# Optimization experiments

Hardware: AMD Instinct MI355X
Metric: run time of the kernel (lower is better)

Reference implementation:

```python
import jax, jax.numpy as jnp
import numpy as np

N_NODES = 100000
N_EDGES = 1600000
H = 64
EPS_SM = 1e-16
NEG_SLOPE = 0.01  # LeakyReLU default
BN_EPS = 1e-5


def leaky_relu(x):
    return jnp.where(x >= 0, x, NEG_SLOPE * x)


def transformer_conv(x, src, tgt, edge_attr, Wq, bq, Wk, bk, Wv, bv, We, Ws, bs):
    # PyG TransformerConv, heads=1, concat=True, root_weight=True, lin_edge bias=False
    n = x.shape[0]
    q = x @ Wq + bq            # [N,H]
    k = x @ Wk + bk            # [N,H]
    v = x @ Wv + bv            # [N,H]
    e = edge_attr @ We         # [E,H]
    ke = k[src] + e            # [E,H]
    score = jnp.sum(q[tgt] * ke, axis=-1) / jnp.sqrt(jnp.float32(H))  # [E]
    # segment softmax over incoming edges of each target node
    m = jax.ops.segment_max(score, tgt, num_segments=n)
    m = jnp.where(jnp.isfinite(m), m, 0.0)
    p = jnp.exp(score - m[tgt])
    denom = jax.ops.segment_sum(p, tgt, num_segments=n)
    alpha = p / (denom[tgt] + EPS_SM)
    msg = (v[src] + e) * alpha[:, None]                  # [E,H]
    out = jax.ops.segment_sum(msg, tgt, num_segments=n)  # [N,H]
    return out + x @ Ws + bs


def batch_norm(x, gamma, beta):
    mean = jnp.mean(x, axis=0)
    var = jnp.mean((x - mean) ** 2, axis=0)
    return (x - mean) / jnp.sqrt(var + BN_EPS) * gamma + beta


def setup_inputs() -> dict:
    key = jax.random.key(0)
    ks = jax.random.split(key, 24)
    s = 0.05
    d = {
        "x": jax.random.normal(ks[0], (N_NODES, 2), jnp.float32),
        "edge_index": jax.random.randint(ks[1], (2, N_EDGES), 0, N_NODES, jnp.int32),
        "edge_attr": jax.random.normal(ks[2], (N_EDGES, 2), jnp.float32),
        "mask": jax.random.uniform(ks[3], (N_NODES,), jnp.float32),
        # gcn1 (in=2)
        "Wq1": jax.random.normal(ks[4], (2, H)) * s, "bq1": jnp.zeros((H,)),
        "Wk1": jax.random.normal(ks[5], (2, H)) * s, "bk1": jnp.zeros((H,)),
        "Wv1": jax.random.normal(ks[6], (2, H)) * s, "bv1": jnp.zeros((H,)),
        "We1": jax.random.normal(ks[7], (2, H)) * s,
        "Ws1": jax.random.normal(ks[8], (2, H)) * s, "bs1": jnp.zeros((H,)),
        # gcn2 (in=64)
        "Wq2": jax.random.normal(ks[9], (H, H)) * s, "bq2": jnp.zeros((H,)),
        "Wk2": jax.random.normal(ks[10], (H, H)) * s, "bk2": jnp.zeros((H,)),
        "Wv2": jax.random.normal(ks[11], (H, H)) * s, "bv2": jnp.zeros((H,)),
        "We2": jax.random.normal(ks[12], (2, H)) * s,
        "Ws2": jax.random.normal(ks[13], (H, H)) * s, "bs2": jnp.zeros((H,)),
        # batch norm
        "bn_gamma": jnp.ones((H,)), "bn_beta": jnp.zeros((H,)),
        # final MLP 64->32->1
        "Wf1": jax.random.normal(ks[14], (H, 32)) * s, "bf1": jnp.zeros((32,)),
        "Wf2": jax.random.normal(ks[15], (32, 1)) * s, "bf2": jnp.zeros((1,)),
        "iterations": 3,
    }
    return d


def reference(x, edge_index, edge_attr, mask,
              Wq1, bq1, Wk1, bk1, Wv1, bv1, We1, Ws1, bs1,
              Wq2, bq2, Wk2, bk2, Wv2, bv2, We2, Ws2, bs2,
              bn_gamma, bn_beta, Wf1, bf1, Wf2, bf2, iterations):
    src, tgt = edge_index[0], edge_index[1]
    h = transformer_conv(x, src, tgt, edge_attr, Wq1, bq1, Wk1, bk1, Wv1, bv1, We1, Ws1, bs1)
    h = leaky_relu(batch_norm(h, bn_gamma, bn_beta))
    h = leaky_relu(transformer_conv(h, src, tgt, edge_attr, Wq2, bq2, Wk2, bk2, Wv2, bv2, We2, Ws2, bs2))
    for _ in range(iterations - 1):
        h = leaky_relu(transformer_conv(h, src, tgt, edge_attr, Wq2, bq2, Wk2, bk2, Wv2, bv2, We2, Ws2, bs2))
    out = jnp.squeeze(leaky_relu(h @ Wf1 + bf1) @ Wf2 + bf2, axis=-1)  # [N]
    return out * mask
```

## Files before the change

### kernel.cpp

```cpp
#include <hip/hip_runtime.h>
#include <hip/hip_fp16.h>

#define N_NODES 100000
#define N_EDGES 1600000
#define SCAN_B ((N_NODES + 1023) / 1024)
#define BSHIFT 7
#define NB_BKT ((N_NODES + 127) / 128)
#define BCAP 2560

typedef _Float16 half2_t __attribute__((ext_vector_type(2)));
typedef _Float16 half8_t __attribute__((ext_vector_type(8)));
typedef float f32x4 __attribute__((ext_vector_type(4)));

__device__ __forceinline__ float lrelu(float x) { return x >= 0.f ? x : 0.01f * x; }

__global__ void k_count(const int* __restrict__ tgt, int* __restrict__ deg) {
    int i = blockIdx.x * 256 + threadIdx.x;
    atomicAdd(&deg[tgt[i]], 1);
}

__global__ void k_scan1(const int* __restrict__ deg, int* __restrict__ bsum) {
    __shared__ int s[256];
    int t = threadIdx.x;
    int gi = blockIdx.x * 1024 + t * 4;
    int v = 0;
    if (gi < N_NODES) {
        int4 d = *(const int4*)&deg[gi];
        v = d.x + d.y + d.z + d.w;
    }
    s[t] = v;
    __syncthreads();
    for (int d = 128; d > 0; d >>= 1) {
        if (t < d) s[t] += s[t + d];
        __syncthreads();
    }
    if (t == 0) bsum[blockIdx.x] = s[0];
}

__global__ void k_scan2(int* bsum, int* rowptr) {
    if (threadIdx.x == 0) {
        int run = 0;
        for (int b = 0; b < SCAN_B; b++) {
            int v = bsum[b];
            bsum[b] = run;
            run += v;
        }
        rowptr[N_NODES] = run;
    }
}

__global__ void k_scan3(const int* __restrict__ deg, const int* __restrict__ bsum,
                        int* __restrict__ rowptr, int* __restrict__ fill) {
    __shared__ int s[256];
    int t = threadIdx.x;
    int gi = blockIdx.x * 1024 + t * 4;
    int4 d = make_int4(0, 0, 0, 0);
    if (gi < N_NODES) d = *(const int4*)&deg[gi];
    int tsum = d.x + d.y + d.z + d.w;
    s[t] = tsum;
    __syncthreads();
    for (int dd = 1; dd < 256; dd <<= 1) {
        int val = (t >= dd) ? s[t - dd] : 0;
        __syncthreads();
        s[t] += val;
        __syncthreads();
    }
    int texcl = s[t] - tsum + bsum[blockIdx.x];
    if (gi < N_NODES) {
        int4 w;
        w.x = texcl;
        w.y = texcl + d.x;
        w.z = texcl + d.x + d.y;
        w.w = texcl + d.x + d.y + d.z;
        *(int4*)&rowptr[gi] = w;
        *(int4*)&fill[gi] = w;
    }
}

__global__ void k_scatter(const int* __restrict__ src, const int* __restrict__ tgt,
                          const float2* __restrict__ ea,
                          int* __restrict__ fill, int2* __restrict__ csr) {
    int i = blockIdx.x * 256 + threadIdx.x;
    int t = tgt[i];
    float2 e = ea[i];
    int pos = atomicAdd(&fill[t], 1);
    __half2 h2 = __floats2half2_rn(e.x, e.y);
    csr[pos] = make_int2(src[i], *(int*)&h2);
}

__global__ __launch_bounds__(256) void k_bin1(const int* __restrict__ src,
                                              const int* __restrict__ tgt,
                                              const float2* __restrict__ ea,
                                              int* __restrict__ gCur,
                                              int2* __restrict__ bin) {
    __shared__ int hist[NB_BKT];
    __shared__ int cur[NB_BKT];
    int tid = threadIdx.x;
    for (int b = tid; b < NB_BKT; b += 256) hist[b] = 0;
    __syncthreads();
    int base = blockIdx.x * 6400;
#pragma unroll 5
    for (int k = 0; k < 25; k++) {
        int i = base + k * 256 + tid;
        atomicAdd(&hist[tgt[i] >> BSHIFT], 1);
    }
    __syncthreads();
    for (int b = tid; b < NB_BKT; b += 256)
        cur[b] = atomicAdd(&gCur[b], hist[b]);
    __syncthreads();
    for (int k = 0; k < 25; k++) {
        int i = base + k * 256 + tid;
        int t = tgt[i];
        int b = t >> BSHIFT;
        float2 e = ea[i];
        int pos = atomicAdd(&cur[b], 1);
        if (pos < BCAP) {
            __half2 h2 = __floats2half2_rn(e.x, e.y);
            int2 rec;
            rec.x = src[i] | ((t & 127) << 20);
            rec.y = *(int*)&h2;
            bin[(size_t)b * BCAP + pos] = rec;
        }
    }
}

__global__ __launch_bounds__(256) void k_bin2(const int* __restrict__ gCnt,
                                              const int2* __restrict__ bin,
                                              int2* __restrict__ csr,
                                              int* __restrict__ fill) {
    __shared__ int cnt[128];
    int tid = threadIdx.x;
    if (tid < 128) cnt[tid] = 0;
    __syncthreads();
    int b = blockIdx.x;
    int nb = min(gCnt[b], BCAP);
    const int2* myb = &bin[(size_t)b * BCAP];
    for (int i = tid; i < nb; i += 256) {
        int2 rec = myb[i];
        int tloc = (rec.x >> 20) & 127;
        int s = rec.x & 0xFFFFF;
        int pos = atomicAdd(&cnt[tloc], 1);
        if (pos < 64) {
            int node = (b << BSHIFT) + tloc;
            csr[((size_t)node << 6) + pos] = make_int2(s | (rec.x & 0xFFF00000), rec.y);
        }
    }
    __syncthreads();
    if (tid < 128) {
        int node = (b << BSHIFT) + tid;
        if (node < N_NODES) fill[node] = min(cnt[tid], 64);
    }
}

__global__ void k_prep2(const float* __restrict__ Wq, const float* __restrict__ Wk,
                        const float* __restrict__ Ws, const float* __restrict__ We,
                        const float* __restrict__ bk, float* __restrict__ Wcomb) {
    int idx = blockIdx.x * 256 + threadIdx.x;
    if (idx >= 9216) return;
    int j = idx / 144;
    int m = idx - j * 144;
    float v = 0.f;
    if (m < 64) {
        float s = 0.f;
        for (int ch = 0; ch < 64; ch++) s += Wq[j * 64 + ch] * Wk[m * 64 + ch];
        v = 0.125f * s;
    } else if (m < 128) {
        v = Ws[j * 64 + (m - 64)];
    } else if (m == 128) {
        float s = 0.f;
        for (int ch = 0; ch < 64; ch++) s += Wq[j * 64 + ch] * bk[ch];
        v = 0.125f * s;
    } else if (m <= 130) {
        float s = 0.f;
        for (int ch = 0; ch < 64; ch++) s += Wq[j * 64 + ch] * We[(m - 129) * 64 + ch];
        v = 0.125f * s;
    }
    Wcomb[idx] = v;
}

__global__ void k_prepb(const float* __restrict__ Wk2, const float* __restrict__ We2,
                        const float* __restrict__ bq2, const float* __restrict__ bk2,
                        const float* __restrict__ bs2, const float* __restrict__ Wq1,
                        const float* __restrict__ Wk1, const float* __restrict__ We1,
                        const float* __restrict__ bq1, const float* __restrict__ bk1,
                        float* __restrict__ bcomb) {
    int t = threadIdx.x;
    if (t >= 160) return;
    float v = 0.f;
    if (t < 64) {
        float s = 0.f;
        for (int i = 0; i < 64; i++) s += Wk2[t * 64 + i] * bq2[i];
        v = 0.125f * s;
    } else if (t < 128) {
        v = bs2[t - 64];
    } else if (t == 128) {
        float s = 0.f;
        for (int i = 0; i < 64; i++) s += bq2[i] * bk2[i];
        v = 0.125f * s;
    } else if (t <= 130) {
        float s = 0.f;
        for (int i = 0; i < 64; i++) s += bq2[i] * We2[(t - 129) * 64 + i];
        v = 0.125f * s;
    } else if (t < 144) {
        v = 0.f;
    } else {
        int t2 = t - 144;
        float s = 0.f;
        if (t2 < 4) {
            int j = t2 >> 1, m = t2 & 1;
            for (int ch = 0; ch < 64; ch++) s += Wq1[j * 64 + ch] * Wk1[m * 64 + ch];
        } else if (t2 < 6) {
            int j = t2 - 4;
            for (int ch = 0; ch < 64; ch++) s += Wq1[j * 64 + ch] * bk1[ch];
        } else if (t2 < 8) {
            int m = t2 - 6;
            for (int ch = 0; ch < 64; ch++) s += bq1[ch] * Wk1[m * 64 + ch];
        } else if (t2 == 8) {
            for (int ch = 0; ch < 64; ch++) s += bq1[ch] * bk1[ch];
        } else if (t2 < 13) {
            int j = (t2 - 9) >> 1, d = (t2 - 9) & 1;
            for (int ch = 0; ch < 64; ch++) s += Wq1[j * 64 + ch] * We1[d * 64 + ch];
        } else if (t2 < 15) {
            int d = t2 - 13;
            for (int ch = 0; ch < 64; ch++) s += bq1[ch] * We1[d * 64 + ch];
        }
        v = 0.125f * s;
    }
    bcomb[t] = v;
}

__global__ void k_prepw(const float* __restrict__ Wcomb, __half* __restrict__ wp) {
    int t = blockIdx.x * 256 + threadIdx.x;
    if (t >= 9216) return;
    int e = t & 7;
    int lane = (t >> 3) & 63;
    int kh = (t >> 9) & 1;
    int fm = t >> 10;
    int k = (kh << 5) + ((lane >> 4) << 3) + e;
    int c = fm * 16 + (lane & 15);
    wp[t] = __float2half(Wcomb[k * 144 + c]);
}

__global__ void k_prepv(const float* __restrict__ Wv, __half* __restrict__ wvp) {
    int t = blockIdx.x * 256 + threadIdx.x;
    if (t >= 4096) return;
    int e = t & 7;
    int lane = (t >> 3) & 63;
    int kh = (t >> 9) & 1;
    int fm = t >> 10;
    int k = (kh << 5) + ((lane >> 4) << 3) + e;
    int c = fm * 16 + (lane & 15);
    wvp[t] = __float2half(Wv[k * 64 + c]);
}

__global__ __launch_bounds__(256) void k_agg1(
    const float* __restrict__ x, const int* __restrict__ idx,
    const int2* __restrict__ csr, const float* __restrict__ Wv,
    const float* __restrict__ We, const float* __restrict__ Ws,
    const float* __restrict__ bv, const float* __restrict__ bs,
    const float* __restrict__ prep, float* __restrict__ o, int bucket) {
    int node = blockIdx.x * 4 + (threadIdx.x >> 6);
    int lane = threadIdx.x & 63;
    float2 xt = *(const float2*)&x[(size_t)node << 1];
    float a0 = xt.x * prep[0] + xt.y * prep[2] + prep[6];
    float a1 = xt.x * prep[1] + xt.y * prep[3] + prep[7];
    float b1 = xt.x * prep[4] + xt.y * prep[5] + prep[8];
    float g0 = xt.x * prep[9] + xt.y * prep[11] + prep[13];
    float g1 = xt.x * prep[10] + xt.y * prep[12] + prep[14];

    float l = 0.f, px0 = 0.f, px1 = 0.f, pA = 0.f, pB = 0.f;
    if (bucket) {
        int deg = idx[node];
        bool valid = lane < deg;
        int2 rec = valid ? csr[((size_t)node << 6) + lane] : make_int2(0, 0);
        int src = rec.x & 0xFFFFF;
        float2 ef = __half22float2(*(__half2*)&rec.y);
        float2 xs = valid ? *(const float2*)&x[(size_t)src << 1] : make_float2(0.f, 0.f);
        float t = a0 * xs.x + a1 * xs.y + b1 + g0 * ef.x + g1 * ef.y;
        float pp = valid ? __expf(t) : 0.f;
        l = pp;
        px0 = pp * xs.x;
        px1 = pp * xs.y;
        pA = pp * ef.x;
        pB = pp * ef.y;
    } else {
        int beg = idx[node], end = idx[node + 1];
        for (int p = beg + lane; p < end; p += 64) {
            int2 rec = csr[p];
            float2 ef = __half22float2(*(__half2*)&rec.y);
            float2 xs = *(const float2*)&x[(size_t)rec.x << 1];
            float t = a0 * xs.x + a1 * xs.y + b1 + g0 * ef.x + g1 * ef.y;
            float pp = __expf(t);
            l += pp;
            px0 += pp * xs.x;
            px1 += pp * xs.y;
            pA += pp * ef.x;
            pB += pp * ef.y;
        }
    }
#pragma unroll
    for (int D = 1; D < 64; D <<= 1) {
        l += __shfl_xor(l, D, 64);
        px0 += __shfl_xor(px0, D, 64);
        px1 += __shfl_xor(px1, D, 64);
        pA += __shfl_xor(pA, D, 64);
        pB += __shfl_xor(pB, D, 64);
    }
    float inv = 1.f / (l + 1e-16f);
    int c = lane;
    float r = (px0 * Wv[c] + px1 * Wv[64 + c] + pA * We[c] + pB * We[64 + c] +
               l * bv[c]) * inv +
              xt.x * Ws[c] + xt.y * Ws[64 + c] + bs[c];
    o[((size_t)node << 6) + c] = r;
}

__global__ void k_bnp(const float* __restrict__ o, float* __restrict__ bnsum,
                      float* __restrict__ bnsq) {
    __shared__ float s1[256], s2[256];
    int t = threadIdx.x;
    int c = t & 63, nsub = t >> 6;
    float su = 0.f, sq = 0.f;
    int base = blockIdx.x * 400;
    for (int i = 0; i < 100; i++) {
        int node = base + i * 4 + nsub;
        float v = o[((size_t)node << 6) + c];
        su += v;
        sq += v * v;
    }
    s1[t] = su;
    s2[t] = sq;
    __syncthreads();
    if (t < 64) {
        float a = s1[t] + s1[t + 64] + s1[t + 128] + s1[t + 192];
        float b = s2[t] + s2[t + 64] + s2[t + 128] + s2[t + 192];
        atomicAdd(&bnsum[t], a);
        atomicAdd(&bnsq[t], b);
    }
}

__global__ void k_bnf(const float* bnsum, const float* bnsq, const float* gamma,
                      const float* beta, float* bnab) {
    int c = threadIdx.x;
    float mean = bnsum[c] * (1.f / N_NODES);
    float var = bnsq[c] * (1.f / N_NODES) - mean * mean;
    float A = gamma[c] * rsqrtf(var + 1e-5f);
    bnab[c] = A;
    bnab[64 + c] = beta[c] - mean * A;
}

__global__ void k_bna(const float* __restrict__ o, const float* __restrict__ bnab,
                      float* __restrict__ h, __half* __restrict__ hh) {
    int idx = blockIdx.x * 256 + threadIdx.x;
    int c = idx & 63;
    float v = lrelu(o[idx] * bnab[c] + bnab[64 + c]);
    h[idx] = v;
    hh[idx] = __float2half(v);
}

__device__ __forceinline__ half8_t pack8(float4 lo, float4 hi) {
    half8_t r;
    r[0] = (_Float16)lo.x; r[1] = (_Float16)lo.y;
    r[2] = (_Float16)lo.z; r[3] = (_Float16)lo.w;
    r[4] = (_Float16)hi.x; r[5] = (_Float16)hi.y;
    r[6] = (_Float16)hi.z; r[7] = (_Float16)hi.w;
    return r;
}

__global__ __launch_bounds__(256) void k_gemm(
    const float* __restrict__ h, const __half* __restrict__ hhin,
    const __half* __restrict__ wp, const float* __restrict__ bcomb,
    const float* __restrict__ bnab, int use_bn,
    __half* __restrict__ qh, float* __restrict__ ext, float* __restrict__ o,
    __half* __restrict__ hhout) {
    int tid = threadIdx.x;
    int w = tid >> 6;
    int lane = tid & 63;
    int nloc = lane & 15;
    int kg = lane >> 4;
    int base = blockIdx.x * 64;
    int fm0 = w << 1;

    half8_t A[2][2], AE[2];
    const half8_t* wpv = (const half8_t*)wp;
#pragma unroll
    for (int fml = 0; fml < 2; fml++)
#pragma unroll
        for (int kh = 0; kh < 2; kh++)
            A[fml][kh] = wpv[(((fm0 + fml) << 1) + kh) * 64 + lane];
    if (w == 3) {
#pragma unroll
        for (int kh = 0; kh < 2; kh++) AE[kh] = wpv[((8 << 1) + kh) * 64 + lane];
    }

    half8_t z8;
#pragma unroll
    for (int i = 0; i < 8; i++) z8[i] = (_Float16)0.f;

    half8_t B[4][2];
    int n[4];
    bool g[4];
#pragma unroll
    for (int nf = 0; nf < 4; nf++) {
        n[nf] = base + (nf << 4) + nloc;
        g[nf] = n[nf] < N_NODES;
    }

    if (use_bn) {
        float4 bnA[2][2], bnB[2][2];
#pragma unroll
        for (int kh = 0; kh < 2; kh++) {
            int k0 = (kh << 5) + (kg << 3);
            bnA[kh][0] = *(const float4*)&bnab[k0];
            bnA[kh][1] = *(const float4*)&bnab[k0 + 4];
            bnB[kh][0] = *(const float4*)&bnab[64 + k0];
            bnB[kh][1] = *(const float4*)&bnab[64 + k0 + 4];
        }
        const float4 z4 = make_float4(0.f, 0.f, 0.f, 0.f);
#pragma unroll
        for (int nf = 0; nf < 4; nf++) {
            const float* hrow = h + ((size_t)n[nf] << 6);
#pragma unroll
            for (int kh = 0; kh < 2; kh++) {
                int k0 = (kh << 5) + (kg << 3);
                float4 lo = g[nf] ? *(const float4*)&hrow[k0] : z4;
                float4 hi = g[nf] ? *(const float4*)&hrow[k0 + 4] : z4;
                lo.x = lrelu(lo.x * bnA[kh][0].x + bnB[kh][0].x);
                lo.y = lrelu(lo.y * bnA[kh][0].y + bnB[kh][0].y);
                lo.z = lrelu(lo.z * bnA[kh][0].z + bnB[kh][0].z);
                lo.w = lrelu(lo.w * bnA[kh][0].w + bnB[kh][0].w);
                hi.x = lrelu(hi.x * bnA[kh][1].x + bnB[kh][1].x);
                hi.y = lrelu(hi.y * bnA[kh][1].y + bnB[kh][1].y);
                hi.z = lrelu(hi.z * bnA[kh][1].z + bnB[kh][1].z);
                hi.w = lrelu(hi.w * bnA[kh][1].w + bnB[kh][1].w);
                B[nf][kh] = pack8(lo, hi);
                if (g[nf]) *(half8_t*)&hhout[((size_t)n[nf] << 6) + k0] = B[nf][kh];
            }
        }
        __syncthreads();
    } else {
#pragma unroll
        for (int nf = 0; nf < 4; nf++) {
#pragma unroll
            for (int kh = 0; kh < 2; kh++) {
                int k0 = (kh << 5) + (kg << 3);
                B[nf][kh] = g[nf] ? *(const half8_t*)&hhin[((size_t)n[nf] << 6) + k0]
                                  : z8;
            }
        }
    }

    f32x4 acc[4][2], accE[4];
#pragma unroll
    for (int nf = 0; nf < 4; nf++) {
        acc[nf][0] = (f32x4){0.f, 0.f, 0.f, 0.f};
        acc[nf][1] = (f32x4){0.f, 0.f, 0.f, 0.f};
        accE[nf] = (f32x4){0.f, 0.f, 0.f, 0.f};
    }

#pragma unroll
    for (int nf = 0; nf < 4; nf++) {
#pragma unroll
        for (int fml = 0; fml < 2; fml++) {
            acc[nf][fml] = __builtin_amdgcn_mfma_f32_16x16x32_f16(
                A[fml][0], B[nf][0], acc[nf][fml], 0, 0, 0);
            acc[nf][fml] = __builtin_amdgcn_mfma_f32_16x16x32_f16(
                A[fml][1], B[nf][1], acc[nf][fml], 0, 0, 0);
        }
    }
    if (w == 3) {
#pragma unroll
        for (int nf = 0; nf < 4; nf++) {
            accE[nf] = __builtin_amdgcn_mfma_f32_16x16x32_f16(AE[0], B[nf][0],
                                                              accE[nf], 0, 0, 0);
            accE[nf] = __builtin_amdgcn_mfma_f32_16x16x32_f16(AE[1], B[nf][1],
                                                              accE[nf], 0, 0, 0);
        }
    }

    int rowg = kg << 2;
#pragma unroll
    for (int fml = 0; fml < 2; fml++) {
        int fm = fm0 + fml;
        float4 bi = *(const float4*)&bcomb[fm * 16 + rowg];
#pragma unroll
        for (int nf = 0; nf < 4; nf++) {
            if (!g[nf]) continue;
            float4 r;
            r.x = acc[nf][fml][0] + bi.x;
            r.y = acc[nf][fml][1] + bi.y;
            r.z = acc[nf][fml][2] + bi.z;
            r.w = acc[nf][fml][3] + bi.w;
            if (fm < 4) {
                __half2 p0 = __floats2half2_rn(r.x, r.y);
                __half2 p1 = __floats2half2_rn(r.z, r.w);
                *(int2*)&qh[((size_t)n[nf] << 6) + fm * 16 + rowg] =
                    make_int2(*(int*)&p0, *(int*)&p1);
            } else {
                *(float4*)&o[((size_t)n[nf] << 6) + (fm - 4) * 16 + rowg] = r;
            }
        }
    }
    if (w == 3 && kg == 0) {
        float4 bi = *(const float4*)&bcomb[128];
#pragma unroll
        for (int nf = 0; nf < 4; nf++) {
            if (!g[nf]) continue;
            float4 r;
            r.x = accE[nf][0] + bi.x;
            r.y = accE[nf][1] + bi.y;
            r.z = accE[nf][2] + bi.z;
            r.w = accE[nf][3] + bi.w;
            *(float4*)&ext[(size_t)n[nf] << 2] = r;
        }
    }
}

__global__ __launch_bounds__(256) void k_aggH(
    const __half* __restrict__ qh, const float* __restrict__ ext,
    const __half* __restrict__ hh, const int* __restrict__ idx,
    const int2* __restrict__ csr, __half* __restrict__ Shat,
    float* __restrict__ svec, int bucket) {
    int tid = threadIdx.x;
    int wv = tid >> 6;
    int node = blockIdx.x * 4 + wv;
    int lane = tid & 63;
    int w = lane >> 4;
    int j = lane & 15;

    float4 ex = *(const float4*)&ext[(size_t)node << 2];
    float beta = ex.x, qe0 = ex.y, qe1 = ex.z;
    int2 qraw = *(const int2*)&qh[((size_t)node << 6) + (j << 2)];
    half2_t q01 = *(half2_t*)&qraw.x;
    half2_t q23 = *(half2_t*)&qraw.y;

    float l = 0.f, sA = 0.f, sB = 0.f;
    float4 acc = make_float4(0.f, 0.f, 0.f, 0.f);

    auto body = [&](int2 hraw, int cry, bool cvalid) {
        float2 ef = __half22float2(*(__half2*)&cry);
#if __has_builtin(__builtin_amdgcn_fdot2)
        half2_t h01 = *(half2_t*)&hraw.x;
        half2_t h23 = *(half2_t*)&hraw.y;
        float t = __builtin_amdgcn_fdot2(h01, q01,
                  __builtin_amdgcn_fdot2(h23, q23, 0.f, false), false);
#else
        float2 a01 = __half22float2(*(__half2*)&hraw.x);
        float2 a23 = __half22float2(*(__half2*)&hraw.y);
        float2 qa = __half22float2(*(__half2*)&qraw.x);
        float2 qb = __half22float2(*(__half2*)&qraw.y);
        float t = qa.x * a01.x + qa.y * a01.y + qb.x * a23.x + qb.y * a23.y;
#endif
#pragma unroll
        for (int off = 1; off < 16; off <<= 1) t += __shfl_xor(t, off, 64);
        t += beta + ef.x * qe0 + ef.y * qe1;
        float pp = cvalid ? __expf(t) : 0.f;
        float2 h01f = __half22float2(*(__half2*)&hraw.x);
        float2 h23f = __half22float2(*(__half2*)&hraw.y);
        l += pp;
        acc.x += pp * h01f.x;
        acc.y += pp * h01f.y;
        acc.z += pp * h23f.x;
        acc.w += pp * h23f.y;
        sA += pp * ef.x;
        sB += pp * ef.y;
    };

    if (bucket) {
        int deg = idx[node];
        int2 myrec = (lane < deg) ? csr[((size_t)node << 6) + lane] : make_int2(0, 0);
        int nIter = (deg + 3) >> 2;
        if (nIter > 0) {
            int es = (w < deg) ? w : 0;
            int rx = __shfl(myrec.x, es, 64) & 0xFFFFF;
            int ry = __shfl(myrec.y, es, 64);
            int2 raw = *(const int2*)&hh[((size_t)rx << 6) + (j << 2)];
            for (int i = 0; i < nIter; i++) {
                int2 craw = raw;
                int cry = ry;
                bool cvalid = (w + (i << 2)) < deg;
                if (i + 1 < nIter) {
                    int e2 = w + ((i + 1) << 2);
                    int es2 = (e2 < deg) ? e2 : 0;
                    rx = __shfl(myrec.x, es2, 64) & 0xFFFFF;
                    ry = __shfl(myrec.y, es2, 64);
                    raw = *(const int2*)&hh[((size_t)rx << 6) + (j << 2)];
                }
                body(craw, cry, cvalid);
            }
        }
    } else {
        int beg = idx[node], end = idx[node + 1];
        for (int p = beg + w; p < end; p += 4) {
            int2 rec = csr[p];
            int2 raw = *(const int2*)&hh[((size_t)rec.x << 6) + (j << 2)];
            body(raw, rec.y, true);
        }
    }

#pragma unroll
    for (int D = 16; D < 64; D <<= 1) {
        l += __shfl_xor(l, D, 64);
        acc.x += __shfl_xor(acc.x, D, 64);
        acc.y += __shfl_xor(acc.y, D, 64);
        acc.z += __shfl_xor(acc.z, D, 64);
        acc.w += __shfl_xor(acc.w, D, 64);
        sA += __shfl_xor(sA, D, 64);
        sB += __shfl_xor(sB, D, 64);
    }

    float inv = 1.f / (l + 1e-16f);
    if (w == 0) {
        __half2 p0 = __floats2half2_rn(acc.x * inv, acc.y * inv);
        __half2 p1 = __floats2half2_rn(acc.z * inv, acc.w * inv);
        *(int2*)&Shat[((size_t)node << 6) + (j << 2)] =
            make_int2(*(int*)&p0, *(int*)&p1);
    }
    if (lane == 0)
        *(float4*)&svec[(size_t)node << 2] =
            make_float4(sA * inv, sB * inv, l * inv, 0.f);
}

__global__ __launch_bounds__(256) void k_proj(
    const __half* __restrict__ Shat, const float* __restrict__ svec,
    const float* __restrict__ skip, const __half* __restrict__ wvp,
    const float* __restrict__ We, const float* __restrict__ bv,
    float* __restrict__ hout, __half* __restrict__ hhout, int whh, int whout) {
    int tid = threadIdx.x;
    int w = tid >> 6;
    int lane = tid & 63;
    int nloc = lane & 15;
    int kg = lane >> 4;
    int base = blockIdx.x * 64;

    const half8_t* wv = (const half8_t*)wvp;
    half8_t A0 = wv[((w << 1) + 0) * 64 + lane];
    half8_t A1 = wv[((w << 1) + 1) * 64 + lane];

    int rowg = kg << 2;
    int c0 = w * 16 + rowg;
    float4 we0 = *(const float4*)&We[c0];
    float4 we1 = *(const float4*)&We[64 + c0];
    float4 bv4 = *(const float4*)&bv[c0];

    half8_t z8;
#pragma unroll
    for (int i = 0; i < 8; i++) z8[i] = (_Float16)0.f;

    int n[4];
    bool g[4];
    half8_t B[4][2];
#pragma unroll
    for (int nf = 0; nf < 4; nf++) {
        n[nf] = base + (nf << 4) + nloc;
        g[nf] = n[nf] < N_NODES;
        const __half* srow = Shat + ((size_t)n[nf] << 6);
        B[nf][0] = g[nf] ? *(const half8_t*)&srow[(kg << 3)] : z8;
        B[nf][1] = g[nf] ? *(const half8_t*)&srow[32 + (kg << 3)] : z8;
    }

    f32x4 acc[4];
#pragma unroll
    for (int nf = 0; nf < 4; nf++) {
        acc[nf] = (f32x4){0.f, 0.f, 0.f, 0.f};
        acc[nf] = __builtin_amdgcn_mfma_f32_16x16x32_f16(A0, B[nf][0], acc[nf],
                                                          0, 0, 0);
        acc[nf] = __builtin_amdgcn_mfma_f32_16x16x32_f16(A1, B[nf][1], acc[nf],
                                                          0, 0, 0);
    }

#pragma unroll
    for (int nf = 0; nf < 4; nf++) {
        if (!g[nf]) continue;
        float4 sv = *(const float4*)&svec[(size_t)n[nf] << 2];
        float4 sk = *(const float4*)&skip[((size_t)n[nf] << 6) + c0];
        float4 r;
        r.x = lrelu(acc[nf][0] + sv.x * we0.x + sv.y * we1.x + sv.z * bv4.x + sk.x);
        r.y = lrelu(acc[nf][1] + sv.x * we0.y + sv.y * we1.y + sv.z * bv4.y + sk.y);
        r.z = lrelu(acc[nf][2] + sv.x * we0.z + sv.y * we1.z + sv.z * bv4.z + sk.z);
        r.w = lrelu(acc[nf][3] + sv.x * we0.w + sv.y * we1.w + sv.z * bv4.w + sk.w);
        if (whout) *(float4*)&hout[((size_t)n[nf] << 6) + c0] = r;
        if (whh) {
            __half2 p0 = __floats2half2_rn(r.x, r.y);
            __half2 p1 = __floats2half2_rn(r.z, r.w);
            *(int2*)&hhout[((size_t)n[nf] << 6) + c0] =
                make_int2(*(int*)&p0, *(int*)&p1);
        }
    }
}

__global__ __launch_bounds__(256) void k_mlp(const float* __restrict__ h,
                                             const float* __restrict__ Wf1,
                                             const float* __restrict__ bf1,
                                             const float* __restrict__ Wf2,
                                             const float* __restrict__ bf2v,
                                             const float* __restrict__ mask,
                                             float* __restrict__ out) {
    __shared__ float W1[64 * 32];
    __shared__ float W2[32];
    __shared__ float hsm[8][64];
    __shared__ float zs[256];
    int tid = threadIdx.x;
    for (int i = tid; i < 2048; i += 256) W1[i] = Wf1[i];
    if (tid < 32) W2[tid] = Wf2[tid];
    int base = blockIdx.x * 8;
    for (int i = tid; i < 512; i += 256) {
        int n = i >> 6, c = i & 63;
        hsm[n][c] = h[(base + n) * 64 + c];
    }
    __syncthreads();
    int n = tid >> 5, j = tid & 31;
    float acc = bf1[j];
    for (int c = 0; c < 64; c++) acc += hsm[n][c] * W1[c * 32 + j];
    zs[tid] = lrelu(acc) * W2[j];
    __syncthreads();
    if (j == 0) {
        int node = base + n;
        float r = bf2v[0];
        for (int jj = 0; jj < 32; jj++) r += zs[(n << 5) + jj];
        out[node] = r * mask[node];
    }
}

extern "C" void kernel_launch(void* const* d_in, const int* in_sizes, int n_in,
                              void* d_out, int out_size, void* d_ws, size_t ws_size,
                              hipStream_t stream) {
    const float* x = (const float*)d_in[0];
    const int* ei = (const int*)d_in[1];
    const float* ea = (const float*)d_in[2];
    const float* mask = (const float*)d_in[3];
    const float *Wq1 = (const float*)d_in[4], *bq1 = (const float*)d_in[5];
    const float *Wk1 = (const float*)d_in[6], *bk1 = (const float*)d_in[7];
    const float *Wv1 = (const float*)d_in[8], *bv1 = (const float*)d_in[9];
    const float *We1 = (const float*)d_in[10];
    const float *Ws1 = (const float*)d_in[11], *bs1 = (const float*)d_in[12];
    const float *Wq2 = (const float*)d_in[13], *bq2 = (const float*)d_in[14];
    const float *Wk2 = (const float*)d_in[15], *bk2 = (const float*)d_in[16];
    const float *Wv2 = (const float*)d_in[17], *bv2 = (const float*)d_in[18];
    const float *We2 = (const float*)d_in[19];
    const float *Ws2 = (const float*)d_in[20], *bs2 = (const float*)d_in[21];
    const float *gamma = (const float*)d_in[22], *beta = (const float*)d_in[23];
    const float *Wf1 = (const float*)d_in[24], *bf1 = (const float*)d_in[25];
    const float *Wf2 = (const float*)d_in[26], *bf2v = (const float*)d_in[27];
    float* out = (float*)d_out;

    const size_t bucket_need =
        (size_t)NB_BKT * BCAP * 8 + (size_t)N_NODES * 64 * 8 +
        (size_t)N_NODES * 64 * 4 * 2 + (size_t)N_NODES * 64 * 2 * 4 +
        (size_t)N_NODES * 16 * 2 + (size_t)N_NODES * 4 * 3 + (1 << 20);
    bool use_bucket = ws_size >= bucket_need;

    char* ws = (char*)d_ws;
    size_t off = 0;
    auto alloc = [&](size_t b) {
        size_t r = off;
        off += (b + 255) & ~(size_t)255;
        return r;
    };
    int* deg = (int*)(ws + alloc(N_NODES * 4));
    int* fill = (int*)(ws + alloc(N_NODES * 4));
    int* rowptr = (int*)(ws + alloc((N_NODES + 1) * 4));
    int* bsum = (int*)(ws + alloc(SCAN_B * 4));
    int* gCur = (int*)(ws + alloc(NB_BKT * 4));
    float* bnsum = (float*)(ws + alloc(64 * 4));
    float* bnsq = (float*)(ws + alloc(64 * 4));
    float* bnab = (float*)(ws + alloc(128 * 4));
    float* Wcomb = (float*)(ws + alloc(9216 * 4));
    float* bcomb = (float*)(ws + alloc(160 * 4));
    __half* wp = (__half*)(ws + alloc(9216 * 2));
    __half* wvp = (__half*)(ws + alloc(4096 * 2));
    float* ext = (float*)(ws + alloc((size_t)N_NODES * 16));
    float* svec = (float*)(ws + alloc((size_t)N_NODES * 16));
    int2* bin1 = (int2*)(ws + alloc(use_bucket ? (size_t)NB_BKT * BCAP * 8 : 256));
    int2* csr = (int2*)(ws + alloc(use_bucket ? (size_t)N_NODES * 64 * 8
                                              : (size_t)N_EDGES * 8));
    __half* qh = (__half*)(ws + alloc((size_t)N_NODES * 64 * 2));
    __half* Shat = (__half*)(ws + alloc((size_t)N_NODES * 64 * 2));
    __half* hh0 = (__half*)(ws + alloc((size_t)N_NODES * 64 * 2));
    __half* hh1 = (__half*)(ws + alloc((size_t)N_NODES * 64 * 2));
    float* hbuf = (float*)(ws + alloc((size_t)N_NODES * 64 * 4));
    float* obuf = (float*)(ws + alloc((size_t)N_NODES * 64 * 4));

    const int* srcI = ei;
    const int* tgtI = ei + N_EDGES;

    hipMemsetAsync(bnsum, 0, 64 * 4, stream);
    hipMemsetAsync(bnsq, 0, 64 * 4, stream);

    k_prep2<<<36, 256, 0, stream>>>(Wq2, Wk2, Ws2, We2, bk2, Wcomb);
    k_prepb<<<1, 192, 0, stream>>>(Wk2, We2, bq2, bk2, bs2, Wq1, Wk1, We1, bq1, bk1,
                                   bcomb);
    k_prepw<<<36, 256, 0, stream>>>(Wcomb, wp);
    k_prepv<<<16, 256, 0, stream>>>(Wv2, wvp);

    const int* aggIdx;
    if (use_bucket) {
        hipMemsetAsync(gCur, 0, NB_BKT * 4, stream);
        k_bin1<<<250, 256, 0, stream>>>(srcI, tgtI, (const float2*)ea, gCur, bin1);
        k_bin2<<<NB_BKT, 256, 0, stream>>>(gCur, bin1, csr, fill);
        aggIdx = fill;
    } else {
        hipMemsetAsync(deg, 0, N_NODES * 4, stream);
        k_count<<<N_EDGES / 256, 256, 0, stream>>>(tgtI, deg);
        k_scan1<<<SCAN_B, 256, 0, stream>>>(deg, bsum);
        k_scan2<<<1, 64, 0, stream>>>(bsum, rowptr);
        k_scan3<<<SCAN_B, 256, 0, stream>>>(deg, bsum, rowptr, fill);
        k_scatter<<<N_EDGES / 256, 256, 0, stream>>>(srcI, tgtI, (const float2*)ea,
                                                     fill, csr);
        aggIdx = rowptr;
    }
    int bkt = use_bucket ? 1 : 0;

    k_agg1<<<N_NODES / 4, 256, 0, stream>>>(x, aggIdx, csr, Wv1, We1, Ws1, bv1, bs1,
                                            bcomb + 144, obuf, bkt);
    k_bnp<<<250, 256, 0, stream>>>(obuf, bnsum, bnsq);
    k_bnf<<<1, 64, 0, stream>>>(bnsum, bnsq, gamma, beta, bnab);
    if (!use_bucket)
        k_bna<<<N_NODES * 64 / 256, 256, 0, stream>>>(obuf, bnab, hbuf, hh0);

    const int gemm_grid = (N_NODES + 63) / 64;
    for (int it = 0; it < 3; ++it) {
        int bnflag = (it == 0 && use_bucket) ? 1 : 0;
        const __half* hhG = (it == 1) ? hh1 : hh0;
        __half* hhP = (it == 0) ? hh1 : hh0;
        k_gemm<<<gemm_grid, 256, 0, stream>>>(obuf, hhG, wp, bcomb, bnab, bnflag,
                                              qh, ext, obuf, (__half*)hhG);
        k_aggH<<<N_NODES / 4, 256, 0, stream>>>(qh, ext, hhG, aggIdx, csr, Shat,
                                                svec, bkt);
        k_proj<<<gemm_grid, 256, 0, stream>>>(Shat, svec, obuf, wvp, We2, bv2,
                                              hbuf, hhP, (it < 2) ? 1 : 0,
                                              (it == 2) ? 1 : 0);
    }
    k_mlp<<<N_NODES / 8, 256, 0, stream>>>(hbuf, Wf1, bf1, Wf2, bf2v, mask, out);
}
```

Before: 577.5 us.

## Move skip projection into k_proj and stage outputs through LDS for coalesced stores

The skip-connection GEMM (x@Ws) is no longer computed in k_gemm and written as an fp32 intermediate. k_proj now recomputes it from the fp16 h copy with two extra MFMAs per fragment, which removes a 25.6MB fp32 write and read per iteration. k_gemm and k_proj now stage their outputs in padded shared memory and write them row-contiguously. k_aggH now writes Shat with all 64 lanes instead of 16. The cost is extra MFMA work, a __syncthreads, and LDS usage in both GEMM kernels.

```diff
diff --git a/kernel.cpp b/kernel.cpp
--- a/kernel.cpp
+++ b/kernel.cpp
@@ -370,23 +370,19 @@
     const float* __restrict__ h, const __half* __restrict__ hhin,
     const __half* __restrict__ wp, const float* __restrict__ bcomb,
     const float* __restrict__ bnab, int use_bn,
-    __half* __restrict__ qh, float* __restrict__ ext, float* __restrict__ o,
-    __half* __restrict__ hhout) {
+    __half* __restrict__ qh, float* __restrict__ ext, __half* __restrict__ hhout) {
+    __shared__ __half qsm[64 * 68];
     int tid = threadIdx.x;
     int w = tid >> 6;
     int lane = tid & 63;
     int nloc = lane & 15;
     int kg = lane >> 4;
     int base = blockIdx.x * 64;
-    int fm0 = w << 1;
-
-    half8_t A[2][2], AE[2];
+
+    half8_t A[2], AE[2];
     const half8_t* wpv = (const half8_t*)wp;
 #pragma unroll
-    for (int fml = 0; fml < 2; fml++)
-#pragma unroll
-        for (int kh = 0; kh < 2; kh++)
-            A[fml][kh] = wpv[(((fm0 + fml) << 1) + kh) * 64 + lane];
+    for (int kh = 0; kh < 2; kh++) A[kh] = wpv[((w << 1) + kh) * 64 + lane];
     if (w == 3) {
 #pragma unroll
         for (int kh = 0; kh < 2; kh++) AE[kh] = wpv[((8 << 1) + kh) * 64 + lane];
@@ -436,7 +432,6 @@
                 if (g[nf]) *(half8_t*)&hhout[((size_t)n[nf] << 6) + k0] = B[nf][kh];
             }
         }
-        __syncthreads();
     } else {
 #pragma unroll
         for (int nf = 0; nf < 4; nf++) {
@@ -449,23 +444,19 @@
         }
     }
 
-    f32x4 acc[4][2], accE[4];
+    f32x4 acc[4], accE[4];
 #pragma unroll
     for (int nf = 0; nf < 4; nf++) {
-        acc[nf][0] = (f32x4){0.f, 0.f, 0.f, 0.f};
-        acc[nf][1] = (f32x4){0.f, 0.f, 0.f, 0.f};
+        acc[nf] = (f32x4){0.f, 0.f, 0.f, 0.f};
         accE[nf] = (f32x4){0.f, 0.f, 0.f, 0.f};
     }
 
 #pragma unroll
     for (int nf = 0; nf < 4; nf++) {
-#pragma unroll
-        for (int fml = 0; fml < 2; fml++) {
-            acc[nf][fml] = __builtin_amdgcn_mfma_f32_16x16x32_f16(
-                A[fml][0], B[nf][0], acc[nf][fml], 0, 0, 0);
-            acc[nf][fml] = __builtin_amdgcn_mfma_f32_16x16x32_f16(
-                A[fml][1], B[nf][1], acc[nf][fml], 0, 0, 0);
-        }
+        acc[nf] = __builtin_amdgcn_mfma_f32_16x16x32_f16(A[0], B[nf][0], acc[nf],
+                                                          0, 0, 0);
+        acc[nf] = __builtin_amdgcn_mfma_f32_16x16x32_f16(A[1], B[nf][1], acc[nf],
+                                                          0, 0, 0);
     }
     if (w == 3) {
 #pragma unroll
@@ -478,39 +469,38 @@
     }
 
     int rowg = kg << 2;
-#pragma unroll
-    for (int fml = 0; fml < 2; fml++) {
-        int fm = fm0 + fml;
-        float4 bi = *(const float4*)&bcomb[fm * 16 + rowg];
+    int c0 = (w << 4) + rowg;
+    float4 bi = *(const float4*)&bcomb[c0];
+#pragma unroll
+    for (int nf = 0; nf < 4; nf++) {
+        int nl = (nf << 4) + nloc;
+        __half2 p0 = __floats2half2_rn(acc[nf][0] + bi.x, acc[nf][1] + bi.y);
+        __half2 p1 = __floats2half2_rn(acc[nf][2] + bi.z, acc[nf][3] + bi.w);
+        *(__half2*)&qsm[nl * 68 + c0] = p0;
+        *(__half2*)&qsm[nl * 68 + c0 + 2] = p1;
+    }
+    if (w == 3 && kg == 0) {
+        float4 be = *(const float4*)&bcomb[128];
 #pragma unroll
         for (int nf = 0; nf < 4; nf++) {
             if (!g[nf]) continue;
             float4 r;
-            r.x = acc[nf][fml][0] + bi.x;
-            r.y = acc[nf][fml][1] + bi.y;
-            r.z = acc[nf][fml][2] + bi.z;
-            r.w = acc[nf][fml][3] + bi.w;
-            if (fm < 4) {
-                __half2 p0 = __floats2half2_rn(r.x, r.y);
-                __half2 p1 = __floats2half2_rn(r.z, r.w);
-                *(int2*)&qh[((size_t)n[nf] << 6) + fm * 16 + rowg] =
-                    make_int2(*(int*)&p0, *(int*)&p1);
-            } else {
-                *(float4*)&o[((size_t)n[nf] << 6) + (fm - 4) * 16 + rowg] = r;
-            }
-        }
-    }
-    if (w == 3 && kg == 0) {
-        float4 bi = *(const float4*)&bcomb[128];
-#pragma unroll
-        for (int nf = 0; nf < 4; nf++) {
-            if (!g[nf]) continue;
-            float4 r;
-            r.x = accE[nf][0] + bi.x;
-            r.y = accE[nf][1] + bi.y;
-            r.z = accE[nf][2] + bi.z;
-            r.w = accE[nf][3] + bi.w;
+            r.x = accE[nf][0] + be.x;
+            r.y = accE[nf][1] + be.y;
+            r.z = accE[nf][2] + be.z;
+            r.w = accE[nf][3] + be.w;
             *(float4*)&ext[(size_t)n[nf] << 2] = r;
+        }
+    }
+    __syncthreads();
+#pragma unroll
+    for (int rep = 0; rep < 8; rep++) {
+        int i = rep * 256 + tid;
+        int row = i >> 5;
+        int col = (i & 31) << 1;
+        if (base + row < N_NODES) {
+            int v = *(int*)&qsm[row * 68 + col];
+            *(int*)&qh[((size_t)(base + row) << 6) + col] = v;
         }
     }
 }
@@ -609,12 +599,13 @@
     }
 
     float inv = 1.f / (l + 1e-16f);
-    if (w == 0) {
-        __half2 p0 = __floats2half2_rn(acc.x * inv, acc.y * inv);
-        __half2 p1 = __floats2half2_rn(acc.z * inv, acc.w * inv);
-        *(int2*)&Shat[((size_t)node << 6) + (j << 2)] =
-            make_int2(*(int*)&p0, *(int*)&p1);
-    }
+    float f0 = __shfl(acc.x * inv, lane >> 2, 64);
+    float f1 = __shfl(acc.y * inv, lane >> 2, 64);
+    float f2 = __shfl(acc.z * inv, lane >> 2, 64);
+    float f3 = __shfl(acc.w * inv, lane >> 2, 64);
+    int sel = lane & 3;
+    float v = (sel == 0) ? f0 : (sel == 1) ? f1 : (sel == 2) ? f2 : f3;
+    Shat[((size_t)node << 6) + lane] = __float2half(v);
     if (lane == 0)
         *(float4*)&svec[(size_t)node << 2] =
             make_float4(sA * inv, sB * inv, l * inv, 0.f);
@@ -622,9 +613,12 @@
 
 __global__ __launch_bounds__(256) void k_proj(
     const __half* __restrict__ Shat, const float* __restrict__ svec,
-    const float* __restrict__ skip, const __half* __restrict__ wvp,
-    const float* __restrict__ We, const float* __restrict__ bv,
+    const __half* __restrict__ hh, const __half* __restrict__ wp,
+    const __half* __restrict__ wvp, const float* __restrict__ We,
+    const float* __restrict__ bv, const float* __restrict__ bcomb,
     float* __restrict__ hout, __half* __restrict__ hhout, int whh, int whout) {
+    __shared__ float lds4[64 * 68];
+    __half* hsm = (__half*)lds4;
     int tid = threadIdx.x;
     int w = tid >> 6;
     int lane = tid & 63;
@@ -633,57 +627,80 @@
     int base = blockIdx.x * 64;
 
     const half8_t* wv = (const half8_t*)wvp;
-    half8_t A0 = wv[((w << 1) + 0) * 64 + lane];
-    half8_t A1 = wv[((w << 1) + 1) * 64 + lane];
+    const half8_t* wpv = (const half8_t*)wp;
+    half8_t Av0 = wv[((w << 1) + 0) * 64 + lane];
+    half8_t Av1 = wv[((w << 1) + 1) * 64 + lane];
+    half8_t As0 = wpv[(((4 + w) << 1) + 0) * 64 + lane];
+    half8_t As1 = wpv[(((4 + w) << 1) + 1) * 64 + lane];
 
     int rowg = kg << 2;
-    int c0 = w * 16 + rowg;
+    int c0 = (w << 4) + rowg;
     float4 we0 = *(const float4*)&We[c0];
     float4 we1 = *(const float4*)&We[64 + c0];
     float4 bv4 = *(const float4*)&bv[c0];
+    float4 bs4 = *(const float4*)&bcomb[64 + c0];
 
     half8_t z8;
 #pragma unroll
     for (int i = 0; i < 8; i++) z8[i] = (_Float16)0.f;
 
-    int n[4];
-    bool g[4];
-    half8_t B[4][2];
 #pragma unroll
     for (int nf = 0; nf < 4; nf++) {
-        n[nf] = base + (nf << 4) + nloc;
-        g[nf] = n[nf] < N_NODES;
-        const __half* srow = Shat + ((size_t)n[nf] << 6);
-        B[nf][0] = g[nf] ? *(const half8_t*)&srow[(kg << 3)] : z8;
-        B[nf][1] = g[nf] ? *(const half8_t*)&srow[32 + (kg << 3)] : z8;
-    }
-
-    f32x4 acc[4];
-#pragma unroll
-    for (int nf = 0; nf < 4; nf++) {
-        acc[nf] = (f32x4){0.f, 0.f, 0.f, 0.f};
-        acc[nf] = __builtin_amdgcn_mfma_f32_16x16x32_f16(A0, B[nf][0], acc[nf],
-                                                          0, 0, 0);
-        acc[nf] = __builtin_amdgcn_mfma_f32_16x16x32_f16(A1, B[nf][1], acc[nf],
-                                                          0, 0, 0);
-    }
-
-#pragma unroll
-    for (int nf = 0; nf < 4; nf++) {
-        if (!g[nf]) continue;
-        float4 sv = *(const float4*)&svec[(size_t)n[nf] << 2];
-        float4 sk = *(const float4*)&skip[((size_t)n[nf] << 6) + c0];
+        int n = base + (nf << 4) + nloc;
+        bool g = n < N_NODES;
+        const __half* srow = Shat + ((size_t)n << 6);
+        const __half* hrow = hh + ((size_t)n << 6);
+        half8_t Bs0 = g ? *(const half8_t*)&srow[(kg << 3)] : z8;
+        half8_t Bs1 = g ? *(const half8_t*)&srow[32 + (kg << 3)] : z8;
+        half8_t Bh0 = g ? *(const half8_t*)&hrow[(kg << 3)] : z8;
+        half8_t Bh1 = g ? *(const half8_t*)&hrow[32 + (kg << 3)] : z8;
+
+        f32x4 acc = (f32x4){0.f, 0.f, 0.f, 0.f};
+        acc = __builtin_amdgcn_mfma_f32_16x16x32_f16(Av0, Bs0, acc, 0, 0, 0);
+        acc = __builtin_amdgcn_mfma_f32_16x16x32_f16(Av1, Bs1, acc, 0, 0, 0);
+        acc = __builtin_amdgcn_mfma_f32_16x16x32_f16(As0, Bh0, acc, 0, 0, 0);
+        acc = __builtin_amdgcn_mfma_f32_16x16x32_f16(As1, Bh1, acc, 0, 0, 0);
+
+        float4 sv = g ? *(const float4*)&svec[(size_t)n << 2]
+                      : make_float4(0.f, 0.f, 0.f, 0.f);
         float4 r;
-        r.x = lrelu(acc[nf][0] + sv.x * we0.x + sv.y * we1.x + sv.z * bv4.x + sk.x);
-        r.y = lrelu(acc[nf][1] + sv.x * we0.y + sv.y * we1.y + sv.z * bv4.y + sk.y);
-        r.z = lrelu(acc[nf][2] + sv.x * we0.z + sv.y * we1.z + sv.z * bv4.z + sk.z);
-        r.w = lrelu(acc[nf][3] + sv.x * we0.w + sv.y * we1.w + sv.z * bv4.w + sk.w);
-        if (whout) *(float4*)&hout[((size_t)n[nf] << 6) + c0] = r;
-        if (whh) {
+        r.x = lrelu(acc[0] + sv.x * we0.x + sv.y * we1.x + sv.z * bv4.x + bs4.x);
+        r.y = lrelu(acc[1] + sv.x * we0.y + sv.y * we1.y + sv.z * bv4.y + bs4.y);
+        r.z = lrelu(acc[2] + sv.x * we0.z + sv.y * we1.z + sv.z * bv4.z + bs4.z);
+        r.w = lrelu(acc[3] + sv.x * we0.w + sv.y * we1.w + sv.z * bv4.w + bs4.w);
+
+        int nl = (nf << 4) + nloc;
+        if (whout) {
+            *(float4*)&lds4[nl * 68 + c0] = r;
+        } else {
             __half2 p0 = __floats2half2_rn(r.x, r.y);
             __half2 p1 = __floats2half2_rn(r.z, r.w);
-            *(int2*)&hhout[((size_t)n[nf] << 6) + c0] =
-                make_int2(*(int*)&p0, *(int*)&p1);
+            *(__half2*)&hsm[nl * 68 + c0] = p0;
+            *(__half2*)&hsm[nl * 68 + c0 + 2] = p1;
+        }
+    }
+    __syncthreads();
+    if (whout) {
+#pragma unroll
+        for (int rep = 0; rep < 4; rep++) {
+            int i = rep * 256 + tid;
+            int row = i >> 4;
+            int c4 = (i & 15) << 2;
+            if (base + row < N_NODES) {
+                float4 v = *(float4*)&lds4[row * 68 + c4];
+                *(float4*)&hout[((size_t)(base + row) << 6) + c4] = v;
+            }
+        }
+    } else {
+#pragma unroll
+        for (int rep = 0; rep < 8; rep++) {
+            int i = rep * 256 + tid;
+            int row = i >> 5;
+            int col = (i & 31) << 1;
+            if (base + row < N_NODES) {
+                int v = *(int*)&hsm[row * 68 + col];
+                *(int*)&hhout[((size_t)(base + row) << 6) + col] = v;
+            }
         }
     }
 }
@@ -823,11 +840,11 @@
         const __half* hhG = (it == 1) ? hh1 : hh0;
         __half* hhP = (it == 0) ? hh1 : hh0;
         k_gemm<<<gemm_grid, 256, 0, stream>>>(obuf, hhG, wp, bcomb, bnab, bnflag,
-                                              qh, ext, obuf, (__half*)hhG);
+                                              qh, ext, (__half*)hhG);
         k_aggH<<<N_NODES / 4, 256, 0, stream>>>(qh, ext, hhG, aggIdx, csr, Shat,
                                                 svec, bkt);
-        k_proj<<<gemm_grid, 256, 0, stream>>>(Shat, svec, obuf, wvp, We2, bv2,
-                                              hbuf, hhP, (it < 2) ? 1 : 0,
+        k_proj<<<gemm_grid, 256, 0, stream>>>(Shat, svec, hhG, wp, wvp, We2, bv2,
+                                              bcomb, hbuf, hhP, (it < 2) ? 1 : 0,
                                               (it == 2) ? 1 : 0);
     }
     k_mlp<<<N_NODES / 8, 256, 0, stream>>>(hbuf, Wf1, bf1, Wf2, bf2v, mask, out);
```

Measured after the change: 570.2 us. No clear change (-1.3%).
